# Optimization experiments

Hardware: AMD Instinct MI355X
Metric: run time of the kernel (lower is better)

Reference implementation:

```python
import jax, jax.numpy as jnp
import numpy as np

N = 131072   # total atoms in flat batch
E = 262144   # total bonds (directed edges)
G = 4096     # number of molecules (graphs)
FN = 30      # atom feature dim
FE = 11      # bond feature dim
H = 256      # hidden_dim
L = 5        # num GINE layers
BN_EPS = 1e-5


def _bn(x, g, b, m, v):
    # BatchNorm1d in eval mode: affine with running stats
    return g * (x - m) * jax.lax.rsqrt(v + BN_EPS) + b


def setup_inputs() -> dict:
    key = jax.random.key(0)
    ks = jax.random.split(key, 48)
    s = 0.05  # weight scale to keep 5-layer residual stack well-conditioned
    inp = {
        'x': jax.random.normal(ks[0], (N, FN), jnp.float32),
        'edge_index': jax.random.randint(ks[1], (2, E), 0, N),
        'batch': jnp.sort(jax.random.randint(ks[2], (N,), 0, G)),
        'edge_attr': jax.random.normal(ks[3], (E, FE), jnp.float32),
        # encoders
        'enc_w': s * jax.random.normal(ks[4], (FN, H), jnp.float32),
        'enc_b': jnp.zeros((H,), jnp.float32),
        'bond_w': s * jax.random.normal(ks[5], (FE, H), jnp.float32),
        'bond_b': jnp.zeros((H,), jnp.float32),
        # per-layer GINE params (stacked over L)
        'eps': jnp.zeros((L,), jnp.float32),
        'w1': s * jax.random.normal(ks[6], (L, H, 2 * H), jnp.float32),
        'b1': jnp.zeros((L, 2 * H), jnp.float32),
        'ibn_g': 1.0 + 0.1 * jax.random.normal(ks[7], (L, 2 * H), jnp.float32),
        'ibn_b': 0.1 * jax.random.normal(ks[8], (L, 2 * H), jnp.float32),
        'ibn_m': 0.1 * jax.random.normal(ks[9], (L, 2 * H), jnp.float32),
        'ibn_v': jnp.ones((L, 2 * H), jnp.float32),
        'w2': s * jax.random.normal(ks[10], (L, 2 * H, H), jnp.float32),
        'b2': jnp.zeros((L, H), jnp.float32),
        'obn_g': 1.0 + 0.1 * jax.random.normal(ks[11], (L, H), jnp.float32),
        'obn_b': 0.1 * jax.random.normal(ks[12], (L, H), jnp.float32),
        'obn_m': 0.1 * jax.random.normal(ks[13], (L, H), jnp.float32),
        'obn_v': jnp.ones((L, H), jnp.float32),
        # classifier
        'cw1': s * jax.random.normal(ks[14], (2 * H, H), jnp.float32),
        'cb1': jnp.zeros((H,), jnp.float32),
        'c1g': 1.0 + 0.1 * jax.random.normal(ks[15], (H,), jnp.float32),
        'c1b': 0.1 * jax.random.normal(ks[16], (H,), jnp.float32),
        'c1m': 0.1 * jax.random.normal(ks[17], (H,), jnp.float32),
        'c1v': jnp.ones((H,), jnp.float32),
        'cw2': s * jax.random.normal(ks[18], (H, H // 2), jnp.float32),
        'cb2': jnp.zeros((H // 2,), jnp.float32),
        'c2g': 1.0 + 0.1 * jax.random.normal(ks[19], (H // 2,), jnp.float32),
        'c2b': 0.1 * jax.random.normal(ks[20], (H // 2,), jnp.float32),
        'c2m': 0.1 * jax.random.normal(ks[21], (H // 2,), jnp.float32),
        'c2v': jnp.ones((H // 2,), jnp.float32),
        'cw3': s * jax.random.normal(ks[22], (H // 2, 1), jnp.float32),
        'cb3': jnp.zeros((1,), jnp.float32),
    }
    return inp


def reference(x, edge_index, batch, edge_attr,
              enc_w, enc_b, bond_w, bond_b,
              eps, w1, b1, ibn_g, ibn_b, ibn_m, ibn_v,
              w2, b2, obn_g, obn_b, obn_m, obn_v,
              cw1, cb1, c1g, c1b, c1m, c1v,
              cw2, cb2, c2g, c2b, c2m, c2v,
              cw3, cb3):
    n = x.shape[0]
    src, dst = edge_index[0], edge_index[1]
    h = x @ enc_w + enc_b                      # [N, H]
    e = edge_attr @ bond_w + bond_b           # [E, H]
    for i in range(L):
        h_in = h
        # GINEConv: (1+eps)*x_i + sum_j relu(x_j + e_ji), then MLP
        msg = jax.nn.relu(h[src] + e)                          # [E, H] gather
        agg = jax.ops.segment_sum(msg, dst, num_segments=n)    # [N, H] scatter-add
        z = (1.0 + eps[i]) * h + agg
        z = jax.nn.relu(_bn(z @ w1[i] + b1[i], ibn_g[i], ibn_b[i], ibn_m[i], ibn_v[i]))
        z = z @ w2[i] + b2[i]
        # outer BN + relu (dropout is identity in eval) + residual
        h = jax.nn.relu(_bn(z, obn_g[i], obn_b[i], obn_m[i], obn_v[i])) + h_in
    # global mean + max pooling by graph id
    counts = jax.ops.segment_sum(jnp.ones((n,), h.dtype), batch, num_segments=G)
    sums = jax.ops.segment_sum(h, batch, num_segments=G)
    mean_p = sums / jnp.maximum(counts, 1.0)[:, None]
    max_p = jax.ops.segment_max(h, batch, num_segments=G)
    max_p = jnp.where(counts[:, None] > 0, max_p, 0.0)
    p = jnp.concatenate([mean_p, max_p], axis=1)               # [G, 2H]
    # classifier (eval mode: dropout off, BN uses running stats)
    q = jax.nn.relu(_bn(p @ cw1 + cb1, c1g, c1b, c1m, c1v))
    q = jax.nn.relu(_bn(q @ cw2 + cb2, c2g, c2b, c2m, c2v))
    out = q @ cw3 + cb3
    return out[:, 0]                                           # [G]
```

## Files before the change

### kernel.cpp

```cpp
#include <hip/hip_runtime.h>
#include <math.h>

#define NA 131072
#define NE 262144
#define NG 4096
#define FN 30
#define FE 11
#define H  256
#define H2 512
#define NL 5
#define BN_EPS 1e-5f
#define KP 32

typedef _Float16 f16x8 __attribute__((ext_vector_type(8)));
typedef _Float16 f16x4 __attribute__((ext_vector_type(4)));
typedef float f32x4 __attribute__((ext_vector_type(4)));

static char* g_buf = nullptr;
__attribute__((constructor)) static void _alloc_private_ws() {
    void* p = nullptr;
    if (hipMalloc(&p, (size_t)320 * 1024 * 1024) == hipSuccess) g_buf = (char*)p;
}

__global__ __launch_bounds__(256) void prep_w_all(const float* __restrict__ w, int K, int N,
                                                  _Float16* __restrict__ hT) {
    const float* wl = w + (size_t)blockIdx.z * K * N;
    _Float16* hTl = hT + (size_t)blockIdx.z * K * N;
    __shared__ float t[32][33];
    const int k0 = blockIdx.x * 32, n0 = blockIdx.y * 32;
    const int tx = threadIdx.x & 31, ty = threadIdx.x >> 5;
    #pragma unroll
    for (int i = 0; i < 4; ++i)
        t[ty + i * 8][tx] = wl[(size_t)(k0 + ty + i * 8) * N + n0 + tx];
    __syncthreads();
    #pragma unroll
    for (int i = 0; i < 4; ++i)
        hTl[(size_t)(n0 + ty + i * 8) * K + k0 + tx] = (_Float16)t[tx][ty + i * 8];
}

__global__ __launch_bounds__(256) void prep_wpad(const float* __restrict__ w, int K_IN,
                                                 _Float16* __restrict__ wT) {
    const int n = threadIdx.x;
    #pragma unroll
    for (int kk = 0; kk < KP / 8; ++kk) {
        f16x8 v;
        #pragma unroll
        for (int j = 0; j < 8; ++j) {
            const int k = kk * 8 + j;
            v[j] = (k < K_IN) ? (_Float16)w[(size_t)k * H + n] : (_Float16)0.0f;
        }
        *(f16x8*)(wT + (size_t)n * KP + kk * 8) = v;
    }
}

__global__ __launch_bounds__(256) void prep_x16(const float* __restrict__ x,
                                                _Float16* __restrict__ x16) {
    const int row = blockIdx.x * 64 + (threadIdx.x >> 2);
    const int g = threadIdx.x & 3;
    f16x8 v;
    #pragma unroll
    for (int j = 0; j < 8; ++j) {
        const int c = g * 8 + j;
        v[j] = (c < FN) ? (_Float16)x[(size_t)row * FN + c] : (_Float16)0.0f;
    }
    *(f16x8*)(x16 + (size_t)row * KP + g * 8) = v;
}

__global__ __launch_bounds__(256) void prep_ea16(const float* __restrict__ eattr,
                                                 const int2* __restrict__ se,
                                                 _Float16* __restrict__ ea16) {
    const int t = blockIdx.x * 64 + (threadIdx.x >> 2);
    const int g = threadIdx.x & 3;
    const int e = se[t].y;
    f16x8 v;
    #pragma unroll
    for (int j = 0; j < 8; ++j) {
        const int c = g * 8 + j;
        v[j] = (c < FE) ? (_Float16)eattr[(size_t)e * FE + c] : (_Float16)0.0f;
    }
    *(f16x8*)(ea16 + (size_t)t * KP + g * 8) = v;
}

__global__ __launch_bounds__(256) void count_deg(const int* __restrict__ ei,
                                                 int* __restrict__ deg) {
    const int e = blockIdx.x * 256 + threadIdx.x;
    if (e < NE) atomicAdd(&deg[ei[NE + e]], 1);
}

__global__ __launch_bounds__(1024) void scan_deg(const int* __restrict__ deg,
                                                 int* __restrict__ rowptr,
                                                 int* __restrict__ cursor) {
    __shared__ int part[1024];
    const int t = threadIdx.x;
    const int base = t * 128;
    int s = 0;
    #pragma unroll 8
    for (int i = 0; i < 128; ++i) s += deg[base + i];
    part[t] = s;
    __syncthreads();
    for (int off = 1; off < 1024; off <<= 1) {
        const int v = (t >= off) ? part[t - off] : 0;
        __syncthreads();
        part[t] += v;
        __syncthreads();
    }
    int run = (t == 0) ? 0 : part[t - 1];
    #pragma unroll 8
    for (int i = 0; i < 128; ++i) {
        rowptr[base + i] = run;
        cursor[base + i] = run;
        run += deg[base + i];
    }
    if (t == 1023) rowptr[NA] = run;
}

__global__ __launch_bounds__(256) void fill_elist(const int* __restrict__ ei,
                                                  int* __restrict__ cursor,
                                                  int2* __restrict__ se) {
    const int e = blockIdx.x * 256 + threadIdx.x;
    if (e < NE) {
        const int src = ei[e];
        const int pos = atomicAdd(&cursor[ei[NE + e]], 1);
        se[pos] = make_int2(src, e);
    }
}

__global__ __launch_bounds__(256) void gine_msg(const _Float16* __restrict__ h16,
                                                const _Float16* __restrict__ eb,
                                                const int2* __restrict__ se,
                                                const int* __restrict__ rowptr,
                                                const float* __restrict__ eps, int l,
                                                _Float16* __restrict__ z) {
    const int dst = blockIdx.x * 4 + (threadIdx.x >> 6);
    const int lane = threadIdx.x & 63;
    const int c = lane * 4;
    const float sc = 1.0f + eps[l];
    const f16x4 hv = *(const f16x4*)(h16 + (size_t)dst * H + c);
    float4 acc;
    acc.x = sc * (float)hv.x; acc.y = sc * (float)hv.y;
    acc.z = sc * (float)hv.z; acc.w = sc * (float)hv.w;
    const int lo = rowptr[dst], hi = rowptr[dst + 1];
    for (int t = lo; t < hi; ++t) {
        const int src = se[t].x;
        const f16x4 hs = *(const f16x4*)(h16 + (size_t)src * H + c);
        const f16x4 ev = *(const f16x4*)(eb + (size_t)t * H + c);
        acc.x += fmaxf((float)hs.x + (float)ev.x, 0.0f);
        acc.y += fmaxf((float)hs.y + (float)ev.y, 0.0f);
        acc.z += fmaxf((float)hs.z + (float)ev.z, 0.0f);
        acc.w += fmaxf((float)hs.w + (float)ev.w, 0.0f);
    }
    f16x4 o;
    o.x = (_Float16)acc.x; o.y = (_Float16)acc.y;
    o.z = (_Float16)acc.z; o.w = (_Float16)acc.w;
    *(f16x4*)(z + (size_t)dst * H + c) = o;
}

__global__ __launch_bounds__(512, 2) void fused_mlp(
    const _Float16* __restrict__ Az,
    const _Float16* __restrict__ W1T,
    const _Float16* __restrict__ W2T,
    const float* __restrict__ b1l, const float* __restrict__ ig,
    const float* __restrict__ ib, const float* __restrict__ im,
    const float* __restrict__ iv,
    const float* __restrict__ b2l, const float* __restrict__ og,
    const float* __restrict__ ob, const float* __restrict__ om,
    const float* __restrict__ ov,
    _Float16* __restrict__ Hio)
{
    __shared__ f16x8 As[2][256];
    __shared__ f16x8 Bs[2][1024];
    __shared__ _Float16 Z1[64 * 520];

    const int tid = threadIdx.x;
    const int m0 = blockIdx.x * 64;
    const int lane = tid & 63, wv = tid >> 6;
    const int lrow = lane & 15, lgrp = lane >> 4;
    const int wm2 = wv >> 2, wn2 = wv & 3;
    const int kq = tid & 3;
    const int brow = tid >> 2;

    f16x8 a_reg, b_reg0, b_reg1;

    #define SLOAD_A(K0) \
        if (tid < 256) a_reg = *(const f16x8*)(Az + (size_t)(m0 + brow) * 256 + (K0) + kq * 8);
    #define SWRITE_A(CUR) \
        if (tid < 256) As[CUR][brow * 4 + (kq ^ ((brow >> 1) & 3))] = a_reg;
    #define SLOAD_B(BASE, K0, KD) { \
        b_reg0 = *(const f16x8*)((BASE) + (size_t)brow * (KD) + (K0) + kq * 8); \
        b_reg1 = *(const f16x8*)((BASE) + (size_t)(brow + 128) * (KD) + (K0) + kq * 8); }
    #define SWRITE_B(CUR) { \
        Bs[CUR][brow * 4 + (kq ^ ((brow >> 1) & 3))] = b_reg0; \
        Bs[CUR][(brow + 128) * 4 + (kq ^ (((brow + 128) >> 1) & 3))] = b_reg1; }

    const f32x4 zero4 = {0.0f, 0.0f, 0.0f, 0.0f};

    #pragma unroll 1
    for (int h = 0; h < 2; ++h) {
        const _Float16* Bb = W1T + (size_t)h * 256 * 256;
        float scl1[4], shf1[4];
        #pragma unroll
        for (int ni = 0; ni < 4; ++ni) {
            const int c = h * 256 + wn2 * 64 + ni * 16 + lrow;
            const float s = ig[c] * rsqrtf(iv[c] + BN_EPS);
            scl1[ni] = s;
            shf1[ni] = s * (b1l[c] - im[c]) + ib[c];
        }
        f32x4 acc[2][4];
        #pragma unroll
        for (int i = 0; i < 2; ++i)
            #pragma unroll
            for (int j = 0; j < 4; ++j) acc[i][j] = zero4;

        SLOAD_A(0); SLOAD_B(Bb, 0, 256);
        int cur = 0;
        #pragma unroll 1
        for (int k0 = 0; k0 < 256; k0 += 32) {
            SWRITE_A(cur); SWRITE_B(cur);
            __syncthreads();
            if (k0 + 32 < 256) { SLOAD_A(k0 + 32); SLOAD_B(Bb, k0 + 32, 256); }
            f16x8 af[2], bf[4];
            #pragma unroll
            for (int mi = 0; mi < 2; ++mi) {
                const int ar = wm2 * 32 + mi * 16 + lrow;
                af[mi] = As[cur][ar * 4 + (lgrp ^ ((ar >> 1) & 3))];
            }
            #pragma unroll
            for (int ni = 0; ni < 4; ++ni) {
                const int br = wn2 * 64 + ni * 16 + lrow;
                bf[ni] = Bs[cur][br * 4 + (lgrp ^ ((br >> 1) & 3))];
            }
            #pragma unroll
            for (int mi = 0; mi < 2; ++mi)
                #pragma unroll
                for (int ni = 0; ni < 4; ++ni)
                    acc[mi][ni] = __builtin_amdgcn_mfma_f32_16x16x32_f16(af[mi], bf[ni], acc[mi][ni], 0, 0, 0);
            cur ^= 1;
        }
        #pragma unroll
        for (int mi = 0; mi < 2; ++mi)
            #pragma unroll
            for (int j = 0; j < 4; ++j) {
                const int row = wm2 * 32 + mi * 16 + lgrp * 4 + j;
                #pragma unroll
                for (int ni = 0; ni < 4; ++ni) {
                    const int col = h * 256 + wn2 * 64 + ni * 16 + lrow;
                    Z1[row * 520 + col] =
                        (_Float16)fmaxf(scl1[ni] * acc[mi][ni][j] + shf1[ni], 0.0f);
                }
            }
        __syncthreads();
    }

    float scl2[4], shf2[4];
    #pragma unroll
    for (int ni = 0; ni < 4; ++ni) {
        const int c = wn2 * 64 + ni * 16 + lrow;
        const float s = og[c] * rsqrtf(ov[c] + BN_EPS);
        scl2[ni] = s;
        shf2[ni] = s * (b2l[c] - om[c]) + ob[c];
    }
    f32x4 acc2[2][4];
    #pragma unroll
    for (int i = 0; i < 2; ++i)
        #pragma unroll
        for (int j = 0; j < 4; ++j) acc2[i][j] = zero4;

    SLOAD_B(W2T, 0, 512);
    int cur = 0;
    #pragma unroll 1
    for (int k0 = 0; k0 < 512; k0 += 32) {
        SWRITE_B(cur);
        __syncthreads();
        if (k0 + 32 < 512) { SLOAD_B(W2T, k0 + 32, 512); }
        f16x8 af[2], bf[4];
        #pragma unroll
        for (int mi = 0; mi < 2; ++mi) {
            const int ar = wm2 * 32 + mi * 16 + lrow;
            af[mi] = *(const f16x8*)&Z1[(size_t)ar * 520 + k0 + lgrp * 8];
        }
        #pragma unroll
        for (int ni = 0; ni < 4; ++ni) {
            const int br = wn2 * 64 + ni * 16 + lrow;
            bf[ni] = Bs[cur][br * 4 + (lgrp ^ ((br >> 1) & 3))];
        }
        #pragma unroll
        for (int mi = 0; mi < 2; ++mi)
            #pragma unroll
            for (int ni = 0; ni < 4; ++ni)
                acc2[mi][ni] = __builtin_amdgcn_mfma_f32_16x16x32_f16(af[mi], bf[ni], acc2[mi][ni], 0, 0, 0);
        cur ^= 1;
    }
    #pragma unroll
    for (int mi = 0; mi < 2; ++mi)
        #pragma unroll
        for (int j = 0; j < 4; ++j) {
            const int row = m0 + wm2 * 32 + mi * 16 + lgrp * 4 + j;
            #pragma unroll
            for (int ni = 0; ni < 4; ++ni) {
                const int col = wn2 * 64 + ni * 16 + lrow;
                float v = fmaxf(scl2[ni] * acc2[mi][ni][j] + shf2[ni], 0.0f);
                v += (float)Hio[(size_t)row * H + col];
                Hio[(size_t)row * H + col] = (_Float16)v;
            }
        }
    #undef SLOAD_A
    #undef SWRITE_A
    #undef SLOAD_B
    #undef SWRITE_B
}

template <int KDIM, int EPI>
__global__ __launch_bounds__(256, 4) void gemm_f16(
    const _Float16* __restrict__ A,
    const _Float16* __restrict__ BT,
    int Ncols,
    const float* __restrict__ bias, const float* __restrict__ bng,
    const float* __restrict__ bnb, const float* __restrict__ bnm,
    const float* __restrict__ bnv,
    _Float16* __restrict__ C16, const _Float16* __restrict__ res)
{
    __shared__ f16x8 As[2][512];
    __shared__ f16x8 Bs[2][512];

    const int tid = threadIdx.x;
    const int nt = Ncols >> 7;
    const int nwg = gridDim.x, orig = blockIdx.x;
    const int q = nwg >> 3, r = nwg & 7;
    const int xcd = orig & 7, rk = orig >> 3;
    const int wg = (xcd < r ? xcd * (q + 1) : r * (q + 1) + (xcd - r) * q) + rk;
    const int m0 = (wg / nt) * 128;
    const int n0 = (wg % nt) * 128;

    const int wid = tid >> 6, lane = tid & 63;
    const int wm = wid >> 1, wn = wid & 1;
    const int lrow = lane & 15, lgrp = lane >> 4;
    const int r0s = tid >> 2;
    const int kq  = tid & 3;
    const int sw0 = kq ^ ((r0s >> 1) & 3);
    const int sw1 = kq ^ (((r0s + 64) >> 1) & 3);

    f32x4 acc[4][4];
    const f32x4 zero4 = {0.0f, 0.0f, 0.0f, 0.0f};
    #pragma unroll
    for (int i = 0; i < 4; ++i)
        #pragma unroll
        for (int j = 0; j < 4; ++j) acc[i][j] = zero4;

    f16x8 a0, a1, b0, b1;
    #define SLOAD(K0)                                                             \
        a0 = *(const f16x8*)(A  + (size_t)(m0 + r0s) * KDIM + (K0) + kq * 8);     \
        a1 = *(const f16x8*)(A  + (size_t)(m0 + r0s + 64) * KDIM + (K0) + kq * 8);\
        b0 = *(const f16x8*)(BT + (size_t)(n0 + r0s) * KDIM + (K0) + kq * 8);     \
        b1 = *(const f16x8*)(BT + (size_t)(n0 + r0s + 64) * KDIM + (K0) + kq * 8);
    #define SWRITE(CUR)                                                           \
        As[CUR][r0s * 4 + sw0] = a0;  As[CUR][(r0s + 64) * 4 + sw1] = a1;         \
        Bs[CUR][r0s * 4 + sw0] = b0;  Bs[CUR][(r0s + 64) * 4 + sw1] = b1;

    SLOAD(0);
    int cur = 0;
    for (int k0 = 0; k0 < KDIM; k0 += 32) {
        SWRITE(cur);
        __syncthreads();
        if (k0 + 32 < KDIM) { SLOAD(k0 + 32); }
        f16x8 af[4], bf[4];
        #pragma unroll
        for (int mi = 0; mi < 4; ++mi) {
            const int ar = wm * 64 + mi * 16 + lrow;
            af[mi] = As[cur][ar * 4 + (lgrp ^ ((ar >> 1) & 3))];
        }
        #pragma unroll
        for (int ni = 0; ni < 4; ++ni) {
            const int br = wn * 64 + ni * 16 + lrow;
            bf[ni] = Bs[cur][br * 4 + (lgrp ^ ((br >> 1) & 3))];
        }
        #pragma unroll
        for (int mi = 0; mi < 4; ++mi)
            #pragma unroll
            for (int ni = 0; ni < 4; ++ni)
                acc[mi][ni] = __builtin_amdgcn_mfma_f32_16x16x32_f16(af[mi], bf[ni], acc[mi][ni], 0, 0, 0);
        cur ^= 1;
    }
    #undef SLOAD
    #undef SWRITE

    float scl[4], shf[4];
    #pragma unroll
    for (int ni = 0; ni < 4; ++ni) {
        const int c = n0 + wn * 64 + ni * 16 + lrow;
        if (EPI == 2) {
            scl[ni] = 1.0f;
            shf[ni] = bias[c];
        } else {
            const float s = bng[c] * rsqrtf(bnv[c] + BN_EPS);
            scl[ni] = s;
            shf[ni] = s * (bias[c] - bnm[c]) + bnb[c];
        }
    }
    #pragma unroll
    for (int mi = 0; mi < 4; ++mi)
        #pragma unroll
        for (int j = 0; j < 4; ++j) {
            const int row = m0 + wm * 64 + mi * 16 + lgrp * 4 + j;
            #pragma unroll
            for (int ni = 0; ni < 4; ++ni) {
                const int col = n0 + wn * 64 + ni * 16 + lrow;
                float v = scl[ni] * acc[mi][ni][j] + shf[ni];
                if (EPI != 2) v = fmaxf(v, 0.0f);
                C16[(size_t)row * Ncols + col] = (_Float16)v;
            }
        }
}

__global__ __launch_bounds__(H) void pool_kernel(const _Float16* __restrict__ h16,
                                                 const int* __restrict__ batch,
                                                 _Float16* __restrict__ p16) {
    const int g = blockIdx.x;
    const int c = threadIdx.x;
    int lo, hi;
    {
        int a = 0, b = NA;
        while (a < b) { int mid = (a + b) >> 1; if (batch[mid] < g) a = mid + 1; else b = mid; }
        lo = a;
        b = NA;
        while (a < b) { int mid = (a + b) >> 1; if (batch[mid] < g + 1) a = mid + 1; else b = mid; }
        hi = a;
    }
    float sum = 0.0f, mx = -INFINITY;
    for (int n = lo; n < hi; ++n) {
        const float v = (float)h16[(size_t)n * H + c];
        sum += v;
        mx = fmaxf(mx, v);
    }
    const int cnt = hi - lo;
    const float mean = (cnt > 0) ? sum / (float)cnt : 0.0f;
    if (cnt == 0) mx = 0.0f;
    p16[(size_t)g * H2 + c] = (_Float16)mean;
    p16[(size_t)g * H2 + H + c] = (_Float16)mx;
}

__global__ __launch_bounds__(64) void final_out(const _Float16* __restrict__ q2,
                                                const float* __restrict__ w,
                                                const float* __restrict__ b,
                                                float* __restrict__ out) {
    const int g = blockIdx.x;
    const int lane = threadIdx.x;
    float acc = (float)q2[(size_t)g * 128 + lane] * w[lane]
              + (float)q2[(size_t)g * 128 + 64 + lane] * w[64 + lane];
    #pragma unroll
    for (int off = 32; off > 0; off >>= 1) acc += __shfl_down(acc, off);
    if (lane == 0) out[g] = acc + b[0];
}

extern "C" void kernel_launch(void* const* d_in, const int* in_sizes, int n_in,
                              void* d_out, int out_size, void* d_ws, size_t ws_size,
                              hipStream_t stream) {
    const float* x      = (const float*)d_in[0];
    const int*   ei     = (const int*)d_in[1];
    const int*   batch  = (const int*)d_in[2];
    const float* eattr  = (const float*)d_in[3];
    const float* enc_w  = (const float*)d_in[4];
    const float* enc_b  = (const float*)d_in[5];
    const float* bond_w = (const float*)d_in[6];
    const float* bond_b = (const float*)d_in[7];
    const float* eps    = (const float*)d_in[8];
    const float* w1     = (const float*)d_in[9];
    const float* b1     = (const float*)d_in[10];
    const float* ibn_g  = (const float*)d_in[11];
    const float* ibn_b  = (const float*)d_in[12];
    const float* ibn_m  = (const float*)d_in[13];
    const float* ibn_v  = (const float*)d_in[14];
    const float* w2     = (const float*)d_in[15];
    const float* b2     = (const float*)d_in[16];
    const float* obn_g  = (const float*)d_in[17];
    const float* obn_b  = (const float*)d_in[18];
    const float* obn_m  = (const float*)d_in[19];
    const float* obn_v  = (const float*)d_in[20];
    const float* cw1    = (const float*)d_in[21];
    const float* cb1    = (const float*)d_in[22];
    const float* c1g    = (const float*)d_in[23];
    const float* c1b    = (const float*)d_in[24];
    const float* c1m    = (const float*)d_in[25];
    const float* c1v    = (const float*)d_in[26];
    const float* cw2    = (const float*)d_in[27];
    const float* cb2    = (const float*)d_in[28];
    const float* c2g    = (const float*)d_in[29];
    const float* c2b    = (const float*)d_in[30];
    const float* c2m    = (const float*)d_in[31];
    const float* c2v    = (const float*)d_in[32];
    const float* cw3    = (const float*)d_in[33];
    const float* cb3    = (const float*)d_in[34];
    float* out = (float*)d_out;

    const size_t WTE       = (size_t)NL * H * H2;
    const size_t CW1E      = (size_t)H2 * H;
    const size_t CW2E      = (size_t)H * (H / 2);
    const size_t EWE       = (size_t)H * KP;
    const size_t BWE       = (size_t)H * KP;
    const size_t wt_bytes  = (2 * WTE + CW1E + CW2E + EWE + BWE) * 2;
    const size_t csr_words = (size_t)3 * NA + 1 + 2 * (size_t)NE + 63;
    const size_t csr_bytes = csr_words * 4;
    const size_t eb_bytes  = (size_t)NE * H * 2;
    const size_t h16_bytes = (size_t)NA * H * 2;
    const size_t z_bytes   = (size_t)NA * H * 2;
    const size_t x16_bytes = (size_t)NA * KP * 2;
    const size_t ea_bytes  = (size_t)NE * KP * 2;
    const size_t need_full = wt_bytes + csr_bytes + eb_bytes + h16_bytes + z_bytes
                           + x16_bytes + ea_bytes;

    char* buf;
    if (ws_size >= need_full) { buf = (char*)d_ws; }
    else if (g_buf)           { buf = g_buf; }
    else                      { buf = (char*)d_ws; }

    _Float16* w1T  = (_Float16*)buf;
    _Float16* w2T  = w1T + WTE;
    _Float16* cw1T = w2T + WTE;
    _Float16* cw2T = cw1T + CW1E;
    _Float16* encT = cw2T + CW2E;
    _Float16* bndT = encT + EWE;
    int*  deg    = (int*)(buf + wt_bytes);
    int*  rowptr = deg + NA;
    int*  cursor = rowptr + NA + 1;
    int2* se     = (int2*)(cursor + NA);
    _Float16* eb  = (_Float16*)(buf + wt_bytes + csr_bytes);
    _Float16* h16 = (_Float16*)((char*)eb + eb_bytes);
    _Float16* z   = (_Float16*)((char*)h16 + h16_bytes);
    _Float16* x16  = (_Float16*)((char*)z + z_bytes);
    _Float16* ea16 = (_Float16*)((char*)x16 + x16_bytes);

    _Float16* p16 = z;
    _Float16* q1  = p16 + (size_t)NG * H2;
    _Float16* q2  = q1 + (size_t)NG * H;

    prep_w_all<<<dim3(H / 32, H2 / 32, NL), 256, 0, stream>>>(w1, H, H2, w1T);
    prep_w_all<<<dim3(H2 / 32, H / 32, NL), 256, 0, stream>>>(w2, H2, H, w2T);
    prep_w_all<<<dim3(H2 / 32, H / 32, 1), 256, 0, stream>>>(cw1, H2, H, cw1T);
    prep_w_all<<<dim3(H / 32, H / 64, 1), 256, 0, stream>>>(cw2, H, H / 2, cw2T);
    prep_wpad<<<1, 256, 0, stream>>>(enc_w, FN, encT);
    prep_wpad<<<1, 256, 0, stream>>>(bond_w, FE, bndT);

    hipMemsetAsync(deg, 0, (size_t)NA * 4, stream);
    count_deg<<<NE / 256, 256, 0, stream>>>(ei, deg);
    scan_deg<<<1, 1024, 0, stream>>>(deg, rowptr, cursor);
    fill_elist<<<NE / 256, 256, 0, stream>>>(ei, cursor, se);

    prep_x16<<<NA / 64, 256, 0, stream>>>(x, x16);
    prep_ea16<<<NE / 64, 256, 0, stream>>>(eattr, se, ea16);

    gemm_f16<KP, 2><<<(NA / 128) * (H / 128), 256, 0, stream>>>(
        x16, encT, H, enc_b, nullptr, nullptr, nullptr, nullptr, h16, nullptr);
    gemm_f16<KP, 2><<<(NE / 128) * (H / 128), 256, 0, stream>>>(
        ea16, bndT, H, bond_b, nullptr, nullptr, nullptr, nullptr, eb, nullptr);

    for (int l = 0; l < NL; ++l) {
        gine_msg<<<NA / 4, 256, 0, stream>>>(h16, eb, se, rowptr, eps, l, z);
        fused_mlp<<<NA / 64, 512, 0, stream>>>(
            z, w1T + (size_t)l * H * H2, w2T + (size_t)l * H2 * H,
            b1 + (size_t)l * H2, ibn_g + (size_t)l * H2, ibn_b + (size_t)l * H2,
            ibn_m + (size_t)l * H2, ibn_v + (size_t)l * H2,
            b2 + (size_t)l * H, obn_g + (size_t)l * H, obn_b + (size_t)l * H,
            obn_m + (size_t)l * H, obn_v + (size_t)l * H,
            h16);
    }

    pool_kernel<<<NG, H, 0, stream>>>(h16, batch, p16);
    gemm_f16<H2, 0><<<(NG / 128) * (H / 128), 256, 0, stream>>>(
        p16, cw1T, H, cb1, c1g, c1b, c1m, c1v, q1, nullptr);
    gemm_f16<H, 0><<<(NG / 128) * ((H / 2) / 128), 256, 0, stream>>>(
        q1, cw2T, H / 2, cb2, c2g, c2b, c2m, c2v, q2, nullptr);
    final_out<<<NG, 64, 0, stream>>>(q2, cw3, cb3, out);
}
```

Baseline: 1.288 ms.

## Hold A tile in registers and deepen B prefetch in fused MLP kernel

The fused MLP kernel now loads each wave's A-operand fragments for the first GEMM straight from global memory into registers once, so the A shared-memory buffer and its per-step stores and loads go away. B tiles are prefetched two steps ahead using two register sets, and both K loops are fully unrolled. Launch bounds drop from 2 to 1 block per CU to make room for the extra registers. This lowers occupancy, so less latency can be hidden across blocks in exchange for fewer LDS round trips.

```diff
diff --git a/kernel.cpp b/kernel.cpp
--- a/kernel.cpp
+++ b/kernel.cpp
@@ -155,7 +155,7 @@
     *(f16x4*)(z + (size_t)dst * H + c) = o;
 }
 
-__global__ __launch_bounds__(512, 2) void fused_mlp(
+__global__ __launch_bounds__(512, 1) void fused_mlp(
     const _Float16* __restrict__ Az,
     const _Float16* __restrict__ W1T,
     const _Float16* __restrict__ W2T,
@@ -167,7 +167,6 @@
     const float* __restrict__ ov,
     _Float16* __restrict__ Hio)
 {
-    __shared__ f16x8 As[2][256];
     __shared__ f16x8 Bs[2][1024];
     __shared__ _Float16 Z1[64 * 520];
 
@@ -178,19 +177,29 @@
     const int wm2 = wv >> 2, wn2 = wv & 3;
     const int kq = tid & 3;
     const int brow = tid >> 2;
-
-    f16x8 a_reg, b_reg0, b_reg1;
-
-    #define SLOAD_A(K0) \
-        if (tid < 256) a_reg = *(const f16x8*)(Az + (size_t)(m0 + brow) * 256 + (K0) + kq * 8);
-    #define SWRITE_A(CUR) \
-        if (tid < 256) As[CUR][brow * 4 + (kq ^ ((brow >> 1) & 3))] = a_reg;
-    #define SLOAD_B(BASE, K0, KD) { \
-        b_reg0 = *(const f16x8*)((BASE) + (size_t)brow * (KD) + (K0) + kq * 8); \
-        b_reg1 = *(const f16x8*)((BASE) + (size_t)(brow + 128) * (KD) + (K0) + kq * 8); }
-    #define SWRITE_B(CUR) { \
-        Bs[CUR][brow * 4 + (kq ^ ((brow >> 1) & 3))] = b_reg0; \
-        Bs[CUR][(brow + 128) * 4 + (kq ^ (((brow + 128) >> 1) & 3))] = b_reg1; }
+    const int bsw0 = brow * 4 + (kq ^ ((brow >> 1) & 3));
+    const int bsw1 = (brow + 128) * 4 + (kq ^ (((brow + 128) >> 1) & 3));
+
+    f16x8 afA0[8], afA1[8];
+    {
+        const int ar0 = m0 + wm2 * 32 + lrow;
+        const int ar1 = ar0 + 16;
+        #pragma unroll
+        for (int ks = 0; ks < 8; ++ks) {
+            afA0[ks] = *(const f16x8*)(Az + (size_t)ar0 * 256 + ks * 32 + lgrp * 8);
+            afA1[ks] = *(const f16x8*)(Az + (size_t)ar1 * 256 + ks * 32 + lgrp * 8);
+        }
+    }
+
+    f16x8 bA0, bB0, bA1, bB1;
+    #define SLOAD_B0(BASE, K0, KD) { \
+        bA0 = *(const f16x8*)((BASE) + (size_t)brow * (KD) + (K0) + kq * 8); \
+        bB0 = *(const f16x8*)((BASE) + (size_t)(brow + 128) * (KD) + (K0) + kq * 8); }
+    #define SLOAD_B1(BASE, K0, KD) { \
+        bA1 = *(const f16x8*)((BASE) + (size_t)brow * (KD) + (K0) + kq * 8); \
+        bB1 = *(const f16x8*)((BASE) + (size_t)(brow + 128) * (KD) + (K0) + kq * 8); }
+    #define SWRITE_B0(CUR) { Bs[CUR][bsw0] = bA0; Bs[CUR][bsw1] = bB0; }
+    #define SWRITE_B1(CUR) { Bs[CUR][bsw0] = bA1; Bs[CUR][bsw1] = bB1; }
 
     const f32x4 zero4 = {0.0f, 0.0f, 0.0f, 0.0f};
 
@@ -211,30 +220,44 @@
             #pragma unroll
             for (int j = 0; j < 4; ++j) acc[i][j] = zero4;
 
-        SLOAD_A(0); SLOAD_B(Bb, 0, 256);
-        int cur = 0;
-        #pragma unroll 1
-        for (int k0 = 0; k0 < 256; k0 += 32) {
-            SWRITE_A(cur); SWRITE_B(cur);
-            __syncthreads();
-            if (k0 + 32 < 256) { SLOAD_A(k0 + 32); SLOAD_B(Bb, k0 + 32, 256); }
-            f16x8 af[2], bf[4];
-            #pragma unroll
-            for (int mi = 0; mi < 2; ++mi) {
-                const int ar = wm2 * 32 + mi * 16 + lrow;
-                af[mi] = As[cur][ar * 4 + (lgrp ^ ((ar >> 1) & 3))];
-            }
-            #pragma unroll
-            for (int ni = 0; ni < 4; ++ni) {
-                const int br = wn2 * 64 + ni * 16 + lrow;
-                bf[ni] = Bs[cur][br * 4 + (lgrp ^ ((br >> 1) & 3))];
-            }
-            #pragma unroll
-            for (int mi = 0; mi < 2; ++mi)
+        SLOAD_B0(Bb, 0, 256);
+        SLOAD_B1(Bb, 32, 256);
+        #pragma unroll
+        for (int kp = 0; kp < 4; ++kp) {
+            {
+                const int cur = 0;
+                SWRITE_B0(cur);
+                __syncthreads();
+                if (kp < 3) SLOAD_B0(Bb, (2 * kp + 2) * 32, 256);
+                f16x8 bf[4];
                 #pragma unroll
-                for (int ni = 0; ni < 4; ++ni)
-                    acc[mi][ni] = __builtin_amdgcn_mfma_f32_16x16x32_f16(af[mi], bf[ni], acc[mi][ni], 0, 0, 0);
-            cur ^= 1;
+                for (int ni = 0; ni < 4; ++ni) {
+                    const int br = wn2 * 64 + ni * 16 + lrow;
+                    bf[ni] = Bs[cur][br * 4 + (lgrp ^ ((br >> 1) & 3))];
+                }
+                #pragma unroll
+                for (int ni = 0; ni < 4; ++ni) {
+                    acc[0][ni] = __builtin_amdgcn_mfma_f32_16x16x32_f16(afA0[2 * kp], bf[ni], acc[0][ni], 0, 0, 0);
+                    acc[1][ni] = __builtin_amdgcn_mfma_f32_16x16x32_f16(afA1[2 * kp], bf[ni], acc[1][ni], 0, 0, 0);
+                }
+            }
+            {
+                const int cur = 1;
+                SWRITE_B1(cur);
+                __syncthreads();
+                if (kp < 3) SLOAD_B1(Bb, (2 * kp + 3) * 32, 256);
+                f16x8 bf[4];
+                #pragma unroll
+                for (int ni = 0; ni < 4; ++ni) {
+                    const int br = wn2 * 64 + ni * 16 + lrow;
+                    bf[ni] = Bs[cur][br * 4 + (lgrp ^ ((br >> 1) & 3))];
+                }
+                #pragma unroll
+                for (int ni = 0; ni < 4; ++ni) {
+                    acc[0][ni] = __builtin_amdgcn_mfma_f32_16x16x32_f16(afA0[2 * kp + 1], bf[ni], acc[0][ni], 0, 0, 0);
+                    acc[1][ni] = __builtin_amdgcn_mfma_f32_16x16x32_f16(afA1[2 * kp + 1], bf[ni], acc[1][ni], 0, 0, 0);
+                }
+            }
         }
         #pragma unroll
         for (int mi = 0; mi < 2; ++mi)
@@ -265,30 +288,56 @@
         #pragma unroll
         for (int j = 0; j < 4; ++j) acc2[i][j] = zero4;
 
-    SLOAD_B(W2T, 0, 512);
-    int cur = 0;
-    #pragma unroll 1
-    for (int k0 = 0; k0 < 512; k0 += 32) {
-        SWRITE_B(cur);
-        __syncthreads();
-        if (k0 + 32 < 512) { SLOAD_B(W2T, k0 + 32, 512); }
-        f16x8 af[2], bf[4];
-        #pragma unroll
-        for (int mi = 0; mi < 2; ++mi) {
-            const int ar = wm2 * 32 + mi * 16 + lrow;
-            af[mi] = *(const f16x8*)&Z1[(size_t)ar * 520 + k0 + lgrp * 8];
-        }
-        #pragma unroll
-        for (int ni = 0; ni < 4; ++ni) {
-            const int br = wn2 * 64 + ni * 16 + lrow;
-            bf[ni] = Bs[cur][br * 4 + (lgrp ^ ((br >> 1) & 3))];
-        }
-        #pragma unroll
-        for (int mi = 0; mi < 2; ++mi)
-            #pragma unroll
-            for (int ni = 0; ni < 4; ++ni)
-                acc2[mi][ni] = __builtin_amdgcn_mfma_f32_16x16x32_f16(af[mi], bf[ni], acc2[mi][ni], 0, 0, 0);
-        cur ^= 1;
+    SLOAD_B0(W2T, 0, 512);
+    SLOAD_B1(W2T, 32, 512);
+    #pragma unroll
+    for (int kp = 0; kp < 8; ++kp) {
+        {
+            const int cur = 0;
+            SWRITE_B0(cur);
+            __syncthreads();
+            if (kp < 7) SLOAD_B0(W2T, (2 * kp + 2) * 32, 512);
+            const int k0 = 2 * kp * 32;
+            f16x8 af[2], bf[4];
+            #pragma unroll
+            for (int mi = 0; mi < 2; ++mi) {
+                const int ar = wm2 * 32 + mi * 16 + lrow;
+                af[mi] = *(const f16x8*)&Z1[(size_t)ar * 520 + k0 + lgrp * 8];
+            }
+            #pragma unroll
+            for (int ni = 0; ni < 4; ++ni) {
+                const int br = wn2 * 64 + ni * 16 + lrow;
+                bf[ni] = Bs[cur][br * 4 + (lgrp ^ ((br >> 1) & 3))];
+            }
+            #pragma unroll
+            for (int mi = 0; mi < 2; ++mi)
+                #pragma unroll
+                for (int ni = 0; ni < 4; ++ni)
+                    acc2[mi][ni] = __builtin_amdgcn_mfma_f32_16x16x32_f16(af[mi], bf[ni], acc2[mi][ni], 0, 0, 0);
+        }
+        {
+            const int cur = 1;
+            SWRITE_B1(cur);
+            __syncthreads();
+            if (kp < 7) SLOAD_B1(W2T, (2 * kp + 3) * 32, 512);
+            const int k0 = (2 * kp + 1) * 32;
+            f16x8 af[2], bf[4];
+            #pragma unroll
+            for (int mi = 0; mi < 2; ++mi) {
+                const int ar = wm2 * 32 + mi * 16 + lrow;
+                af[mi] = *(const f16x8*)&Z1[(size_t)ar * 520 + k0 + lgrp * 8];
+            }
+            #pragma unroll
+            for (int ni = 0; ni < 4; ++ni) {
+                const int br = wn2 * 64 + ni * 16 + lrow;
+                bf[ni] = Bs[cur][br * 4 + (lgrp ^ ((br >> 1) & 3))];
+            }
+            #pragma unroll
+            for (int mi = 0; mi < 2; ++mi)
+                #pragma unroll
+                for (int ni = 0; ni < 4; ++ni)
+                    acc2[mi][ni] = __builtin_amdgcn_mfma_f32_16x16x32_f16(af[mi], bf[ni], acc2[mi][ni], 0, 0, 0);
+        }
     }
     #pragma unroll
     for (int mi = 0; mi < 2; ++mi)
@@ -303,10 +352,10 @@
                 Hio[(size_t)row * H + col] = (_Float16)v;
             }
         }
-    #undef SLOAD_A
-    #undef SWRITE_A
-    #undef SLOAD_B
-    #undef SWRITE_B
+    #undef SLOAD_B0
+    #undef SLOAD_B1
+    #undef SWRITE_B0
+    #undef SWRITE_B1
 }
 
 template <int KDIM, int EPI>
```

Measured after the change: 1.288 ms. About the same (-0.0%).
